# Kernel optimization log

Measured on AMD Instinct MI355X. Metric: run time of the kernel, lower is better.

## Reference

```python
import jax, jax.numpy as jnp
import numpy as np

B, D, H = 512, 256, 512

def setup_inputs() -> dict:
    key = jax.random.key(0)
    ks = jax.random.split(key, 7)
    s = lambda fan_in: 1.0 / np.sqrt(fan_in)
    return {
        "h": jax.random.normal(ks[0], (B, D), jnp.float32),
        "W1": jax.random.normal(ks[1], (2 * D, H), jnp.float32) * s(2 * D),
        "b1": jax.random.normal(ks[2], (H,), jnp.float32) * s(2 * D),
        "W2": jax.random.normal(ks[3], (H, H), jnp.float32) * s(H),
        "b2": jax.random.normal(ks[4], (H,), jnp.float32) * s(H),
        "W3": jax.random.normal(ks[5], (H, 1), jnp.float32) * s(H),
        "b3": jax.random.normal(ks[6], (1,), jnp.float32) * s(H),
    }

def reference(h, W1, b1, W2, b2, W3, b3):
    n = h.shape[0]
    # Split W1 into halves acting on hi and hj; equivalent to cat([hi,hj]) @ W1
    yi = h @ W1[:D]            # [B, H]
    yj = h @ W1[D:]            # [B, H]
    x = jnp.tanh(yi[:, None, :] + yj[None, :, :] + b1)   # [B, B, H]
    x = jnp.tanh(x @ W2 + b2)                             # [B, B, H]
    logits = (x @ W3 + b3)[..., 0]                        # [B, B]
    eye = jnp.eye(n, dtype=logits.dtype)
    return logits * (1.0 - eye) + (-20.0) * eye
```

## Files before the change

kernel.cpp:

```cpp
#include <hip/hip_runtime.h>
#include <hip/hip_bf16.h>
#include <cstdint>


#define NB 512
#define ND 256
#define NH 512
#define C2 2.885390081777927f

typedef int i32x4 __attribute__((ext_vector_type(4)));
typedef int i32x16 __attribute__((ext_vector_type(16)));
typedef unsigned int u32;
typedef unsigned char u8;

__device__ __forceinline__ float exp2_fast(float x) {
#if __has_builtin(__builtin_amdgcn_exp2f)
  return __builtin_amdgcn_exp2f(x);
#else
  return exp2f(x);
#endif
}
__device__ __forceinline__ float rcp_fast(float x) {
#if __has_builtin(__builtin_amdgcn_rcpf)
  return __builtin_amdgcn_rcpf(x);
#else
  return 1.0f / x;
#endif
}
__device__ __forceinline__ u32 perm_b32(u32 hi, u32 lo, u32 sel) {
#if __has_builtin(__builtin_amdgcn_perm)
  return __builtin_amdgcn_perm(hi, lo, sel);
#else
  u32 r = 0;
  for (int b = 0; b < 4; ++b) {
    const u32 c = (sel >> (8 * b)) & 255;
    const u32 byte = (c < 4) ? (lo >> (8 * c)) & 255 : (c < 8) ? (hi >> (8 * (c - 4))) & 255 : 0;
    r |= byte << (8 * b);
  }
  return r;
#endif
}
__device__ __forceinline__ u32 tanh_q127_magic(float u) {
  const float r = rcp_fast(exp2_fast(u) + 1.0f);
  return __builtin_bit_cast(u32, fmaf(-254.0f, r, 12583039.0f));
}

__global__ __launch_bounds__(256) void prep_all(const float* __restrict__ h,
                                                const float* __restrict__ W1,
                                                const float* __restrict__ b1,
                                                const float* __restrict__ W2,
                                                float* __restrict__ Ai,
                                                float* __restrict__ Aj,
                                                u8* __restrict__ W2q) {
  const int t = threadIdx.x;
  const int bx = blockIdx.x;
  if (bx < 1024) {
    __shared__ float hsh[ND];
    const int i = bx >> 1;
    const int n = (bx & 1) * 256 + t;
    hsh[t] = h[i * ND + t];
    __syncthreads();
    float ai = 0.0f, aj = 0.0f;
#pragma unroll 8
    for (int d = 0; d < ND; ++d) {
      const float hd = hsh[d];
      ai = fmaf(hd, W1[d * NH + n], ai);
      aj = fmaf(hd, W1[(d + ND) * NH + n], aj);
    }
    Ai[i * NH + n] = ai * C2;
    Aj[i * NH + n] = (aj + b1[n]) * C2;
  } else {
    const int g = (bx - 1024) * 256 + t;
    const int lane = g & 63;
    const int nt = (g >> 6) & 15;
    const int ks = g >> 10;
    const int n = nt * 32 + (lane & 31);
    const int kb = ks * 32 + ((lane >> 5) << 4);
    u32 w[4];
#pragma unroll
    for (int q = 0; q < 4; ++q) {
      u32 acc = 0;
#pragma unroll
      for (int j = 0; j < 4; ++j) {
        const float wv = fminf(fmaxf(W2[(kb + q * 4 + j) * NH + n], -0.25f), 0.25f);
        const int qi = (int)rintf(wv * 508.0f);
        acc |= ((u32)(qi & 255)) << (8 * j);
      }
      w[q] = acc;
    }
    ((uint4*)W2q)[g] = make_uint4(w[0], w[1], w[2], w[3]);
  }
}

__global__ __launch_bounds__(512, 6) void pair_main(const float* __restrict__ Ai,
                                                    const float* __restrict__ Aj,
                                                    const u8* __restrict__ W2q,
                                                    const float* __restrict__ b2,
                                                    const float* __restrict__ W3,
                                                    const float* __restrict__ b3,
                                                    float* __restrict__ out) {
  __shared__ __align__(16) u8 xs[32 * 512];
  __shared__ float red[8][32];

  const int t = threadIdx.x;
  const int w = t >> 6;
  const int lane = t & 63;
  const int lhi = lane >> 5;
  const int llo = lane & 31;
  const int bx = blockIdx.x;
  const int i = bx >> 4;
  const int j0 = (bx & 15) * 32;

  i32x16 acc[2];
#pragma unroll
  for (int nt = 0; nt < 2; ++nt)
#pragma unroll
    for (int q = 0; q < 16; ++q) acc[nt][q] = 0;

  {
    const int row = t & 31;
    const int s0 = t >> 5;
    const float* ajr = Aj + (size_t)(j0 + row) * NH;
    const float* air = Ai + (size_t)i * NH;
#pragma unroll
    for (int uu = 0; uu < 2; ++uu) {
      const int s = s0 + uu * 16;
      const int k0 = s * 16;
      u32 wds[4];
#pragma unroll
      for (int q = 0; q < 4; ++q) {
        const float4 fa = *(const float4*)(ajr + k0 + q * 4);
        const float4 ga = *(const float4*)(air + k0 + q * 4);
        const u32 m0 = tanh_q127_magic(fa.x + ga.x);
        const u32 m1 = tanh_q127_magic(fa.y + ga.y);
        const u32 m2 = tanh_q127_magic(fa.z + ga.z);
        const u32 m3 = tanh_q127_magic(fa.w + ga.w);
        const u32 p01 = perm_b32(m1, m0, 0x0C0C0400u);
        const u32 p23 = perm_b32(m3, m2, 0x0C0C0400u);
        wds[q] = perm_b32(p23, p01, 0x05040100u);
      }
      ((uint4*)xs)[s * 32 + row] = make_uint4(wds[0], wds[1], wds[2], wds[3]);
    }
  }
  __syncthreads();

  const i32x4* xsv = (const i32x4*)xs;
  const int abase = lhi * 32 + llo;
  const uint4* w2v = (const uint4*)W2q + w * 128 + lane;

  i32x4 aP0 = xsv[abase];
  i32x4 aP1 = xsv[64 + abase];
  uint4 bP00 = w2v[0], bP01 = w2v[64];
  uint4 bP10 = w2v[1024], bP11 = w2v[1024 + 64];

#pragma unroll
  for (int kk = 0; kk < 8; ++kk) {
    const int ks0 = 2 * kk;
    {
      const i32x4 a = aP0;
      const i32x4 c0 = __builtin_bit_cast(i32x4, bP00);
      const i32x4 c1 = __builtin_bit_cast(i32x4, bP01);
      if (kk < 7) {
        aP0 = xsv[(ks0 + 2) * 64 + abase];
        const uint4* wp = w2v + (ks0 + 2) * 1024;
        bP00 = wp[0];
        bP01 = wp[64];
      }
      acc[0] = __builtin_amdgcn_mfma_i32_32x32x32_i8(a, c0, acc[0], 0, 0, 0);
      acc[1] = __builtin_amdgcn_mfma_i32_32x32x32_i8(a, c1, acc[1], 0, 0, 0);
    }
    {
      const i32x4 a = aP1;
      const i32x4 c0 = __builtin_bit_cast(i32x4, bP10);
      const i32x4 c1 = __builtin_bit_cast(i32x4, bP11);
      if (kk < 7) {
        aP1 = xsv[(ks0 + 3) * 64 + abase];
        const uint4* wp = w2v + (ks0 + 3) * 1024;
        bP10 = wp[0];
        bP11 = wp[64];
      }
      acc[0] = __builtin_amdgcn_mfma_i32_32x32x32_i8(a, c0, acc[0], 0, 0, 0);
      acc[1] = __builtin_amdgcn_mfma_i32_32x32x32_i8(a, c1, acc[1], 0, 0, 0);
    }
  }

  const float SCALE = (0.25f / (127.0f * 127.0f)) * C2;
  float b2c[2], w3v[2];
#pragma unroll
  for (int ntl = 0; ntl < 2; ++ntl) {
    const int n = w * 64 + ntl * 32 + llo;
    b2c[ntl] = b2[n] * C2;
    w3v[ntl] = W3[n];
  }
  float w3s = w3v[0] + w3v[1];
#pragma unroll
  for (int off = 1; off < 32; off <<= 1) w3s += __shfl_xor(w3s, off, 64);

#pragma unroll
  for (int reg = 0; reg < 16; ++reg) {
    float sr = 0.0f;
#pragma unroll
    for (int ntl = 0; ntl < 2; ++ntl) {
      const float y = fmaf((float)acc[ntl][reg], SCALE, b2c[ntl]);
      const float r = rcp_fast(exp2_fast(y) + 1.0f);
      sr = fmaf(w3v[ntl], r, sr);
    }
#pragma unroll
    for (int off = 1; off < 32; off <<= 1) sr += __shfl_xor(sr, off, 64);
    const int row = (reg & 3) + 8 * (reg >> 2) + 4 * lhi;
    if (llo == reg) red[w][row] = fmaf(-2.0f, sr, w3s);
  }
  __syncthreads();
  if (t < 32) {
    float v = b3[0];
#pragma unroll
    for (int ww = 0; ww < 8; ++ww) v += red[ww][t];
    const int j = j0 + t;
    out[i * NB + j] = (j == i) ? -20.0f : v;
  }
}

extern "C" void kernel_launch(void* const* d_in, const int* in_sizes, int n_in,
                              void* d_out, int out_size, void* d_ws, size_t ws_size,
                              hipStream_t stream) {
  const float* h = (const float*)d_in[0];
  const float* W1 = (const float*)d_in[1];
  const float* b1 = (const float*)d_in[2];
  const float* W2 = (const float*)d_in[3];
  const float* b2 = (const float*)d_in[4];
  const float* W3 = (const float*)d_in[5];
  const float* b3 = (const float*)d_in[6];
  float* out = (float*)d_out;

  float* Ai = (float*)d_ws;
  float* Aj = Ai + NB * NH;
  u8* W2q = (u8*)(Aj + NB * NH);

  prep_all<<<1088, 256, 0, stream>>>(h, W1, b1, W2, Ai, Aj, W2q);
  pair_main<<<8192, 512, 0, stream>>>(Ai, Aj, W2q, b2, W3, b3, out);
}
```

Before: 233.6 us.

## Enlarge pair tiles to 64 rows and batch four rows in W1 prep

pair_main now uses 1024-thread blocks that each cover 64 j-rows. Two groups of 8 waves share the same W2q column slices, which halves the grid and the per-block overhead. prep_all computes four h rows per block so each W1 element loaded is reused four times. The larger blocks raise the LDS per block and the launch bounds may pressure registers, which could lower occupancy or cause spills.

```diff
diff --git a/kernel.cpp b/kernel.cpp
--- a/kernel.cpp
+++ b/kernel.cpp
@@ -1,5 +1,4 @@
 #include <hip/hip_runtime.h>
-#include <hip/hip_bf16.h>
 #include <cstdint>
 
 
@@ -54,23 +53,34 @@
                                                 u8* __restrict__ W2q) {
   const int t = threadIdx.x;
   const int bx = blockIdx.x;
-  if (bx < 1024) {
-    __shared__ float hsh[ND];
-    const int i = bx >> 1;
+  if (bx < 256) {
+    __shared__ float hsh[4][ND];
+    const int i0 = (bx >> 1) * 4;
     const int n = (bx & 1) * 256 + t;
-    hsh[t] = h[i * ND + t];
+#pragma unroll
+    for (int ii = 0; ii < 4; ++ii) hsh[ii][t] = h[(i0 + ii) * ND + t];
     __syncthreads();
-    float ai = 0.0f, aj = 0.0f;
-#pragma unroll 8
+    float ai[4] = {0.0f, 0.0f, 0.0f, 0.0f};
+    float aj[4] = {0.0f, 0.0f, 0.0f, 0.0f};
+#pragma unroll 4
     for (int d = 0; d < ND; ++d) {
-      const float hd = hsh[d];
-      ai = fmaf(hd, W1[d * NH + n], ai);
-      aj = fmaf(hd, W1[(d + ND) * NH + n], aj);
-    }
-    Ai[i * NH + n] = ai * C2;
-    Aj[i * NH + n] = (aj + b1[n]) * C2;
+      const float wa = W1[d * NH + n];
+      const float wb = W1[(d + ND) * NH + n];
+#pragma unroll
+      for (int ii = 0; ii < 4; ++ii) {
+        const float hd = hsh[ii][d];
+        ai[ii] = fmaf(hd, wa, ai[ii]);
+        aj[ii] = fmaf(hd, wb, aj[ii]);
+      }
+    }
+    const float b1n = b1[n];
+#pragma unroll
+    for (int ii = 0; ii < 4; ++ii) {
+      Ai[(i0 + ii) * NH + n] = ai[ii] * C2;
+      Aj[(i0 + ii) * NH + n] = (aj[ii] + b1n) * C2;
+    }
   } else {
-    const int g = (bx - 1024) * 256 + t;
+    const int g = (bx - 256) * 256 + t;
     const int lane = g & 63;
     const int nt = (g >> 6) & 15;
     const int ks = g >> 10;
@@ -92,24 +102,26 @@
   }
 }
 
-__global__ __launch_bounds__(512, 6) void pair_main(const float* __restrict__ Ai,
-                                                    const float* __restrict__ Aj,
-                                                    const u8* __restrict__ W2q,
-                                                    const float* __restrict__ b2,
-                                                    const float* __restrict__ W3,
-                                                    const float* __restrict__ b3,
-                                                    float* __restrict__ out) {
-  __shared__ __align__(16) u8 xs[32 * 512];
-  __shared__ float red[8][32];
+__global__ __launch_bounds__(1024, 8) void pair_main(const float* __restrict__ Ai,
+                                                     const float* __restrict__ Aj,
+                                                     const u8* __restrict__ W2q,
+                                                     const float* __restrict__ b2,
+                                                     const float* __restrict__ W3,
+                                                     const float* __restrict__ b3,
+                                                     float* __restrict__ out) {
+  __shared__ __align__(16) u8 xs[64 * 512];
+  __shared__ float red[16][32];
 
   const int t = threadIdx.x;
   const int w = t >> 6;
   const int lane = t & 63;
   const int lhi = lane >> 5;
   const int llo = lane & 31;
+  const int wn = w & 7;
+  const int mh = w >> 3;
   const int bx = blockIdx.x;
-  const int i = bx >> 4;
-  const int j0 = (bx & 15) * 32;
+  const int i = bx >> 3;
+  const int j0 = (bx & 7) * 64;
 
   i32x16 acc[2];
 #pragma unroll
@@ -118,8 +130,8 @@
     for (int q = 0; q < 16; ++q) acc[nt][q] = 0;
 
   {
-    const int row = t & 31;
-    const int s0 = t >> 5;
+    const int row = t & 63;
+    const int s0 = t >> 6;
     const float* ajr = Aj + (size_t)(j0 + row) * NH;
     const float* air = Ai + (size_t)i * NH;
 #pragma unroll
@@ -139,17 +151,17 @@
         const u32 p23 = perm_b32(m3, m2, 0x0C0C0400u);
         wds[q] = perm_b32(p23, p01, 0x05040100u);
       }
-      ((uint4*)xs)[s * 32 + row] = make_uint4(wds[0], wds[1], wds[2], wds[3]);
+      ((uint4*)xs)[s * 64 + row] = make_uint4(wds[0], wds[1], wds[2], wds[3]);
     }
   }
   __syncthreads();
 
   const i32x4* xsv = (const i32x4*)xs;
-  const int abase = lhi * 32 + llo;
-  const uint4* w2v = (const uint4*)W2q + w * 128 + lane;
+  const int abase = lhi * 64 + mh * 32 + llo;
+  const uint4* w2v = (const uint4*)W2q + wn * 128 + lane;
 
   i32x4 aP0 = xsv[abase];
-  i32x4 aP1 = xsv[64 + abase];
+  i32x4 aP1 = xsv[128 + abase];
   uint4 bP00 = w2v[0], bP01 = w2v[64];
   uint4 bP10 = w2v[1024], bP11 = w2v[1024 + 64];
 
@@ -161,7 +173,7 @@
       const i32x4 c0 = __builtin_bit_cast(i32x4, bP00);
       const i32x4 c1 = __builtin_bit_cast(i32x4, bP01);
       if (kk < 7) {
-        aP0 = xsv[(ks0 + 2) * 64 + abase];
+        aP0 = xsv[(ks0 + 2) * 128 + abase];
         const uint4* wp = w2v + (ks0 + 2) * 1024;
         bP00 = wp[0];
         bP01 = wp[64];
@@ -174,7 +186,7 @@
       const i32x4 c0 = __builtin_bit_cast(i32x4, bP10);
       const i32x4 c1 = __builtin_bit_cast(i32x4, bP11);
       if (kk < 7) {
-        aP1 = xsv[(ks0 + 3) * 64 + abase];
+        aP1 = xsv[(ks0 + 3) * 128 + abase];
         const uint4* wp = w2v + (ks0 + 3) * 1024;
         bP10 = wp[0];
         bP11 = wp[64];
@@ -188,7 +200,7 @@
   float b2c[2], w3v[2];
 #pragma unroll
   for (int ntl = 0; ntl < 2; ++ntl) {
-    const int n = w * 64 + ntl * 32 + llo;
+    const int n = wn * 64 + ntl * 32 + llo;
     b2c[ntl] = b2[n] * C2;
     w3v[ntl] = W3[n];
   }
@@ -211,10 +223,12 @@
     if (llo == reg) red[w][row] = fmaf(-2.0f, sr, w3s);
   }
   __syncthreads();
-  if (t < 32) {
+  if (t < 64) {
+    const int mh2 = t >> 5;
+    const int rl = t & 31;
     float v = b3[0];
 #pragma unroll
-    for (int ww = 0; ww < 8; ++ww) v += red[ww][t];
+    for (int ww = 0; ww < 8; ++ww) v += red[mh2 * 8 + ww][rl];
     const int j = j0 + t;
     out[i * NB + j] = (j == i) ? -20.0f : v;
   }
@@ -236,6 +250,6 @@
   float* Aj = Ai + NB * NH;
   u8* W2q = (u8*)(Aj + NB * NH);
 
-  prep_all<<<1088, 256, 0, stream>>>(h, W1, b1, W2, Ai, Aj, W2q);
-  pair_main<<<8192, 512, 0, stream>>>(Ai, Aj, W2q, b2, W3, b3, out);
-}
+  prep_all<<<320, 256, 0, stream>>>(h, W1, b1, W2, Ai, Aj, W2q);
+  pair_main<<<4096, 1024, 0, stream>>>(Ai, Aj, W2q, b2, W3, b3, out);
+}
```

Result: slower. 248.2 us (+6.3%).

## Make pair kernel persistent per row with double-buffered tanh tile overlap

Applied to the files above, without the earlier changes.

Each pair_main block now owns one row i and loops over all 16 column tiles. The tanh quantization of the next tile's activations is computed and written into a second shared-memory buffer, interleaved with the current tile's int8 MFMA steps, with Aj rows prefetched into registers. The reduction output is also double-buffered to drop one barrier per tile. The prep kernel's W1 projection becomes a shared-memory tiled GEMM (16 rows by 32 columns per block), which raises W1 reuse. The trade-off is a grid cut from 8192 to 512 blocks, lower occupancy bounds and higher register pressure, so latency hiding depends on the intra-block overlap.

```diff
diff --git a/kernel.cpp b/kernel.cpp
--- a/kernel.cpp
+++ b/kernel.cpp
@@ -1,5 +1,4 @@
 #include <hip/hip_runtime.h>
-#include <hip/hip_bf16.h>
 #include <cstdint>
 
 
@@ -54,23 +53,59 @@
                                                 u8* __restrict__ W2q) {
   const int t = threadIdx.x;
   const int bx = blockIdx.x;
-  if (bx < 1024) {
-    __shared__ float hsh[ND];
-    const int i = bx >> 1;
-    const int n = (bx & 1) * 256 + t;
-    hsh[t] = h[i * ND + t];
-    __syncthreads();
-    float ai = 0.0f, aj = 0.0f;
-#pragma unroll 8
-    for (int d = 0; d < ND; ++d) {
-      const float hd = hsh[d];
-      ai = fmaf(hd, W1[d * NH + n], ai);
-      aj = fmaf(hd, W1[(d + ND) * NH + n], aj);
-    }
-    Ai[i * NH + n] = ai * C2;
-    Aj[i * NH + n] = (aj + b1[n]) * C2;
+  if (bx < 512) {
+    __shared__ float hs[16][68];
+    __shared__ float w1t[64][36];
+    __shared__ float w1b[64][36];
+    const int it = bx >> 4, nt = bx & 15;
+    const int i0 = it * 16, n0 = nt * 32;
+    const int nn = t & 31, ig = t >> 5;
+    float accA[2] = {0.f, 0.f}, accB[2] = {0.f, 0.f};
+    for (int c2 = 0; c2 < 4; ++c2) {
+      __syncthreads();
+      {
+        const int r = t >> 4, c0 = (t & 15) * 4;
+        *(float4*)&hs[r][c0] = *(const float4*)(h + (size_t)(i0 + r) * ND + c2 * 64 + c0);
+      }
+      {
+        const int r = t >> 2, c0 = (t & 3) * 8;
+        const float* st = W1 + (size_t)(c2 * 64 + r) * NH + n0 + c0;
+        const float* sb = W1 + (size_t)(256 + c2 * 64 + r) * NH + n0 + c0;
+        const float4 a = *(const float4*)st;
+        const float4 b = *(const float4*)(st + 4);
+        const float4 c = *(const float4*)sb;
+        const float4 d = *(const float4*)(sb + 4);
+        *(float4*)&w1t[r][c0] = a;
+        *(float4*)&w1t[r][c0 + 4] = b;
+        *(float4*)&w1b[r][c0] = c;
+        *(float4*)&w1b[r][c0 + 4] = d;
+      }
+      __syncthreads();
+#pragma unroll 4
+      for (int k4 = 0; k4 < 16; ++k4) {
+        const float4 hv0 = *(const float4*)&hs[ig * 2 + 0][k4 * 4];
+        const float4 hv1 = *(const float4*)&hs[ig * 2 + 1][k4 * 4];
+        const float* h0 = (const float*)&hv0;
+        const float* h1 = (const float*)&hv1;
+#pragma unroll
+        for (int j = 0; j < 4; ++j) {
+          const float wtj = w1t[k4 * 4 + j][nn];
+          const float wbj = w1b[k4 * 4 + j][nn];
+          accA[0] = fmaf(h0[j], wtj, accA[0]);
+          accA[1] = fmaf(h1[j], wtj, accA[1]);
+          accB[0] = fmaf(h0[j], wbj, accB[0]);
+          accB[1] = fmaf(h1[j], wbj, accB[1]);
+        }
+      }
+    }
+    const float b1n = b1[n0 + nn];
+#pragma unroll
+    for (int r = 0; r < 2; ++r) {
+      Ai[(size_t)(i0 + ig * 2 + r) * NH + n0 + nn] = accA[r] * C2;
+      Aj[(size_t)(i0 + ig * 2 + r) * NH + n0 + nn] = (accB[r] + b1n) * C2;
+    }
   } else {
-    const int g = (bx - 1024) * 256 + t;
+    const int g = (bx - 512) * 256 + t;
     const int lane = g & 63;
     const int nt = (g >> 6) & 15;
     const int ks = g >> 10;
@@ -92,40 +127,45 @@
   }
 }
 
-__global__ __launch_bounds__(512, 6) void pair_main(const float* __restrict__ Ai,
+__global__ __launch_bounds__(512, 4) void pair_main(const float* __restrict__ Ai,
                                                     const float* __restrict__ Aj,
                                                     const u8* __restrict__ W2q,
                                                     const float* __restrict__ b2,
                                                     const float* __restrict__ W3,
                                                     const float* __restrict__ b3,
                                                     float* __restrict__ out) {
-  __shared__ __align__(16) u8 xs[32 * 512];
-  __shared__ float red[8][32];
+  __shared__ __align__(16) u8 xs[2][32 * 512];
+  __shared__ float red[2][8][32];
 
   const int t = threadIdx.x;
   const int w = t >> 6;
   const int lane = t & 63;
   const int lhi = lane >> 5;
   const int llo = lane & 31;
-  const int bx = blockIdx.x;
-  const int i = bx >> 4;
-  const int j0 = (bx & 15) * 32;
-
-  i32x16 acc[2];
-#pragma unroll
-  for (int nt = 0; nt < 2; ++nt)
-#pragma unroll
-    for (int q = 0; q < 16; ++q) acc[nt][q] = 0;
+  const int i = blockIdx.x;
+
+  const int srow = t & 31;
+  const int ss0 = t >> 5;
+  const float* air = Ai + (size_t)i * NH;
+
+  const float SCALE = (0.25f / (127.0f * 127.0f)) * C2;
+  float b2c[2], w3v[2];
+#pragma unroll
+  for (int ntl = 0; ntl < 2; ++ntl) {
+    const int n = w * 64 + ntl * 32 + llo;
+    b2c[ntl] = b2[n] * C2;
+    w3v[ntl] = W3[n];
+  }
+  float w3s = w3v[0] + w3v[1];
+#pragma unroll
+  for (int off = 1; off < 32; off <<= 1) w3s += __shfl_xor(w3s, off, 64);
+  const float b3v = b3[0];
 
   {
-    const int row = t & 31;
-    const int s0 = t >> 5;
-    const float* ajr = Aj + (size_t)(j0 + row) * NH;
-    const float* air = Ai + (size_t)i * NH;
+    const float* ajr = Aj + (size_t)srow * NH;
 #pragma unroll
     for (int uu = 0; uu < 2; ++uu) {
-      const int s = s0 + uu * 16;
-      const int k0 = s * 16;
+      const int k0 = ss0 * 16 + uu * 256;
       u32 wds[4];
 #pragma unroll
       for (int q = 0; q < 4; ++q) {
@@ -139,84 +179,126 @@
         const u32 p23 = perm_b32(m3, m2, 0x0C0C0400u);
         wds[q] = perm_b32(p23, p01, 0x05040100u);
       }
-      ((uint4*)xs)[s * 32 + row] = make_uint4(wds[0], wds[1], wds[2], wds[3]);
+      ((uint4*)xs[0])[(ss0 + uu * 16) * 32 + srow] = make_uint4(wds[0], wds[1], wds[2], wds[3]);
+    }
+  }
+  float4 fjv[8];
+  {
+    const float* ajn = Aj + (size_t)(32 + srow) * NH;
+#pragma unroll
+    for (int g = 0; g < 8; ++g) {
+      const int koff = ss0 * 16 + (g >> 2) * 256 + (g & 3) * 4;
+      fjv[g] = *(const float4*)(ajn + koff);
     }
   }
   __syncthreads();
 
-  const i32x4* xsv = (const i32x4*)xs;
   const int abase = lhi * 32 + llo;
   const uint4* w2v = (const uint4*)W2q + w * 128 + lane;
 
-  i32x4 aP0 = xsv[abase];
-  i32x4 aP1 = xsv[64 + abase];
-  uint4 bP00 = w2v[0], bP01 = w2v[64];
-  uint4 bP10 = w2v[1024], bP11 = w2v[1024 + 64];
-
-#pragma unroll
-  for (int kk = 0; kk < 8; ++kk) {
-    const int ks0 = 2 * kk;
-    {
-      const i32x4 a = aP0;
-      const i32x4 c0 = __builtin_bit_cast(i32x4, bP00);
-      const i32x4 c1 = __builtin_bit_cast(i32x4, bP01);
-      if (kk < 7) {
-        aP0 = xsv[(ks0 + 2) * 64 + abase];
-        const uint4* wp = w2v + (ks0 + 2) * 1024;
-        bP00 = wp[0];
-        bP01 = wp[64];
-      }
-      acc[0] = __builtin_amdgcn_mfma_i32_32x32x32_i8(a, c0, acc[0], 0, 0, 0);
-      acc[1] = __builtin_amdgcn_mfma_i32_32x32x32_i8(a, c1, acc[1], 0, 0, 0);
-    }
-    {
-      const i32x4 a = aP1;
-      const i32x4 c0 = __builtin_bit_cast(i32x4, bP10);
-      const i32x4 c1 = __builtin_bit_cast(i32x4, bP11);
-      if (kk < 7) {
-        aP1 = xsv[(ks0 + 3) * 64 + abase];
-        const uint4* wp = w2v + (ks0 + 3) * 1024;
-        bP10 = wp[0];
-        bP11 = wp[64];
-      }
-      acc[0] = __builtin_amdgcn_mfma_i32_32x32x32_i8(a, c0, acc[0], 0, 0, 0);
-      acc[1] = __builtin_amdgcn_mfma_i32_32x32x32_i8(a, c1, acc[1], 0, 0, 0);
-    }
-  }
-
-  const float SCALE = (0.25f / (127.0f * 127.0f)) * C2;
-  float b2c[2], w3v[2];
-#pragma unroll
-  for (int ntl = 0; ntl < 2; ++ntl) {
-    const int n = w * 64 + ntl * 32 + llo;
-    b2c[ntl] = b2[n] * C2;
-    w3v[ntl] = W3[n];
-  }
-  float w3s = w3v[0] + w3v[1];
-#pragma unroll
-  for (int off = 1; off < 32; off <<= 1) w3s += __shfl_xor(w3s, off, 64);
-
-#pragma unroll
-  for (int reg = 0; reg < 16; ++reg) {
-    float sr = 0.0f;
-#pragma unroll
-    for (int ntl = 0; ntl < 2; ++ntl) {
-      const float y = fmaf((float)acc[ntl][reg], SCALE, b2c[ntl]);
-      const float r = rcp_fast(exp2_fast(y) + 1.0f);
-      sr = fmaf(w3v[ntl], r, sr);
-    }
-#pragma unroll
-    for (int off = 1; off < 32; off <<= 1) sr += __shfl_xor(sr, off, 64);
-    const int row = (reg & 3) + 8 * (reg >> 2) + 4 * lhi;
-    if (llo == reg) red[w][row] = fmaf(-2.0f, sr, w3s);
-  }
-  __syncthreads();
+#pragma unroll 1
+  for (int p = 0; p < 16; ++p) {
+    const i32x4* xsv = (const i32x4*)xs[p & 1];
+    u8* xsw = xs[(p + 1) & 1];
+    const bool notlast = (p < 15);
+
+    i32x16 acc[2];
+#pragma unroll
+    for (int nt = 0; nt < 2; ++nt)
+#pragma unroll
+      for (int q = 0; q < 16; ++q) acc[nt][q] = 0;
+
+    i32x4 aP0 = xsv[abase];
+    i32x4 aP1 = xsv[64 + abase];
+    uint4 bP00 = w2v[0], bP01 = w2v[64];
+    uint4 bP10 = w2v[1024], bP11 = w2v[1024 + 64];
+
+    u32 wd[8];
+#pragma unroll
+    for (int kk = 0; kk < 8; ++kk) {
+      const int ks0 = 2 * kk;
+      {
+        const i32x4 a = aP0;
+        const i32x4 c0 = __builtin_bit_cast(i32x4, bP00);
+        const i32x4 c1 = __builtin_bit_cast(i32x4, bP01);
+        if (kk < 7) {
+          aP0 = xsv[(ks0 + 2) * 64 + abase];
+          const uint4* wp = w2v + (ks0 + 2) * 1024;
+          bP00 = wp[0];
+          bP01 = wp[64];
+        }
+        acc[0] = __builtin_amdgcn_mfma_i32_32x32x32_i8(a, c0, acc[0], 0, 0, 0);
+        acc[1] = __builtin_amdgcn_mfma_i32_32x32x32_i8(a, c1, acc[1], 0, 0, 0);
+      }
+      if (notlast) {
+        const int koff = ss0 * 16 + (kk >> 2) * 256 + (kk & 3) * 4;
+        const float4 ga = *(const float4*)(air + koff);
+        const float4 fa = fjv[kk];
+        const u32 m0 = tanh_q127_magic(fa.x + ga.x);
+        const u32 m1 = tanh_q127_magic(fa.y + ga.y);
+        const u32 m2 = tanh_q127_magic(fa.z + ga.z);
+        const u32 m3 = tanh_q127_magic(fa.w + ga.w);
+        const u32 p01 = perm_b32(m1, m0, 0x0C0C0400u);
+        const u32 p23 = perm_b32(m3, m2, 0x0C0C0400u);
+        wd[kk] = perm_b32(p23, p01, 0x05040100u);
+        if (kk == 3) ((uint4*)xsw)[ss0 * 32 + srow] = make_uint4(wd[0], wd[1], wd[2], wd[3]);
+        if (kk == 7) ((uint4*)xsw)[(ss0 + 16) * 32 + srow] = make_uint4(wd[4], wd[5], wd[6], wd[7]);
+      }
+      {
+        const i32x4 a = aP1;
+        const i32x4 c0 = __builtin_bit_cast(i32x4, bP10);
+        const i32x4 c1 = __builtin_bit_cast(i32x4, bP11);
+        if (kk < 7) {
+          aP1 = xsv[(ks0 + 3) * 64 + abase];
+          const uint4* wp = w2v + (ks0 + 3) * 1024;
+          bP10 = wp[0];
+          bP11 = wp[64];
+        }
+        acc[0] = __builtin_amdgcn_mfma_i32_32x32x32_i8(a, c0, acc[0], 0, 0, 0);
+        acc[1] = __builtin_amdgcn_mfma_i32_32x32x32_i8(a, c1, acc[1], 0, 0, 0);
+      }
+    }
+
+    if (p < 14) {
+      const float* ajn = Aj + (size_t)((p + 2) * 32 + srow) * NH;
+#pragma unroll
+      for (int g = 0; g < 8; ++g) {
+        const int koff = ss0 * 16 + (g >> 2) * 256 + (g & 3) * 4;
+        fjv[g] = *(const float4*)(ajn + koff);
+      }
+    }
+
+#pragma unroll
+    for (int reg = 0; reg < 16; ++reg) {
+      float sr = 0.0f;
+#pragma unroll
+      for (int ntl = 0; ntl < 2; ++ntl) {
+        const float y = fmaf((float)acc[ntl][reg], SCALE, b2c[ntl]);
+        const float r = rcp_fast(exp2_fast(y) + 1.0f);
+        sr = fmaf(w3v[ntl], r, sr);
+      }
+#pragma unroll
+      for (int off = 1; off < 32; off <<= 1) sr += __shfl_xor(sr, off, 64);
+      const int row = (reg & 3) + 8 * (reg >> 2) + 4 * lhi;
+      if (llo == reg) red[p & 1][w][row] = fmaf(-2.0f, sr, w3s);
+    }
+
+    if (p > 0 && t < 32) {
+      float v = b3v;
+#pragma unroll
+      for (int ww = 0; ww < 8; ++ww) v += red[(p & 1) ^ 1][ww][t];
+      const int jp = (p - 1) * 32 + t;
+      out[i * NB + jp] = (jp == i) ? -20.0f : v;
+    }
+    __syncthreads();
+  }
+
   if (t < 32) {
-    float v = b3[0];
-#pragma unroll
-    for (int ww = 0; ww < 8; ++ww) v += red[ww][t];
-    const int j = j0 + t;
-    out[i * NB + j] = (j == i) ? -20.0f : v;
+    float v = b3v;
+#pragma unroll
+    for (int ww = 0; ww < 8; ++ww) v += red[1][ww][t];
+    const int jp = 480 + t;
+    out[i * NB + jp] = (jp == i) ? -20.0f : v;
   }
 }
 
@@ -236,6 +318,6 @@
   float* Aj = Ai + NB * NH;
   u8* W2q = (u8*)(Aj + NB * NH);
 
-  prep_all<<<1088, 256, 0, stream>>>(h, W1, b1, W2, Ai, Aj, W2q);
-  pair_main<<<8192, 512, 0, stream>>>(Ai, Aj, W2q, b2, W3, b3, out);
-}
+  prep_all<<<576, 256, 0, stream>>>(h, W1, b1, W2, Ai, Aj, W2q);
+  pair_main<<<512, 512, 0, stream>>>(Ai, Aj, W2q, b2, W3, b3, out);
+}
```

After: 430.1 us. 84.1% more time.

## Tile first-layer projection in prep kernel with shared-memory staging of h and W1

Applied to the files above, without the earlier changes.

Replaces the per-row projection, where each block streamed all of W1 from global memory for a single input row, with a tiled GEMM. Each block now computes a 16x32 output tile and stages h and both W1 halves through shared memory in 64-wide K chunks. This cuts global W1 traffic by reusing each loaded weight across 16 rows, and halves the number of prep blocks. The prep kernel is small next to pair_main, so the effect on total time is limited.

```diff
diff --git a/kernel.cpp b/kernel.cpp
--- a/kernel.cpp
+++ b/kernel.cpp
@@ -1,5 +1,4 @@
 #include <hip/hip_runtime.h>
-#include <hip/hip_bf16.h>
 #include <cstdint>
 
 
@@ -54,23 +53,59 @@
                                                 u8* __restrict__ W2q) {
   const int t = threadIdx.x;
   const int bx = blockIdx.x;
-  if (bx < 1024) {
-    __shared__ float hsh[ND];
-    const int i = bx >> 1;
-    const int n = (bx & 1) * 256 + t;
-    hsh[t] = h[i * ND + t];
-    __syncthreads();
-    float ai = 0.0f, aj = 0.0f;
-#pragma unroll 8
-    for (int d = 0; d < ND; ++d) {
-      const float hd = hsh[d];
-      ai = fmaf(hd, W1[d * NH + n], ai);
-      aj = fmaf(hd, W1[(d + ND) * NH + n], aj);
-    }
-    Ai[i * NH + n] = ai * C2;
-    Aj[i * NH + n] = (aj + b1[n]) * C2;
+  if (bx < 512) {
+    __shared__ float hs[16][68];
+    __shared__ float w1t[64][36];
+    __shared__ float w1b[64][36];
+    const int it = bx >> 4, nt = bx & 15;
+    const int i0 = it * 16, n0 = nt * 32;
+    const int nn = t & 31, ig = t >> 5;
+    float accA[2] = {0.f, 0.f}, accB[2] = {0.f, 0.f};
+    for (int c2 = 0; c2 < 4; ++c2) {
+      __syncthreads();
+      {
+        const int r = t >> 4, c0 = (t & 15) * 4;
+        *(float4*)&hs[r][c0] = *(const float4*)(h + (size_t)(i0 + r) * ND + c2 * 64 + c0);
+      }
+      {
+        const int r = t >> 2, c0 = (t & 3) * 8;
+        const float* st = W1 + (size_t)(c2 * 64 + r) * NH + n0 + c0;
+        const float* sb = W1 + (size_t)(256 + c2 * 64 + r) * NH + n0 + c0;
+        const float4 a = *(const float4*)st;
+        const float4 b = *(const float4*)(st + 4);
+        const float4 c = *(const float4*)sb;
+        const float4 d = *(const float4*)(sb + 4);
+        *(float4*)&w1t[r][c0] = a;
+        *(float4*)&w1t[r][c0 + 4] = b;
+        *(float4*)&w1b[r][c0] = c;
+        *(float4*)&w1b[r][c0 + 4] = d;
+      }
+      __syncthreads();
+#pragma unroll 4
+      for (int k4 = 0; k4 < 16; ++k4) {
+        const float4 hv0 = *(const float4*)&hs[ig * 2 + 0][k4 * 4];
+        const float4 hv1 = *(const float4*)&hs[ig * 2 + 1][k4 * 4];
+        const float* h0 = (const float*)&hv0;
+        const float* h1 = (const float*)&hv1;
+#pragma unroll
+        for (int j = 0; j < 4; ++j) {
+          const float wtj = w1t[k4 * 4 + j][nn];
+          const float wbj = w1b[k4 * 4 + j][nn];
+          accA[0] = fmaf(h0[j], wtj, accA[0]);
+          accA[1] = fmaf(h1[j], wtj, accA[1]);
+          accB[0] = fmaf(h0[j], wbj, accB[0]);
+          accB[1] = fmaf(h1[j], wbj, accB[1]);
+        }
+      }
+    }
+    const float b1n = b1[n0 + nn];
+#pragma unroll
+    for (int r = 0; r < 2; ++r) {
+      Ai[(size_t)(i0 + ig * 2 + r) * NH + n0 + nn] = accA[r] * C2;
+      Aj[(size_t)(i0 + ig * 2 + r) * NH + n0 + nn] = (accB[r] + b1n) * C2;
+    }
   } else {
-    const int g = (bx - 1024) * 256 + t;
+    const int g = (bx - 512) * 256 + t;
     const int lane = g & 63;
     const int nt = (g >> 6) & 15;
     const int ks = g >> 10;
@@ -236,6 +271,6 @@
   float* Aj = Ai + NB * NH;
   u8* W2q = (u8*)(Aj + NB * NH);
 
-  prep_all<<<1088, 256, 0, stream>>>(h, W1, b1, W2, Ai, Aj, W2q);
+  prep_all<<<576, 256, 0, stream>>>(h, W1, b1, W2, Ai, Aj, W2q);
   pair_main<<<8192, 512, 0, stream>>>(Ai, Aj, W2q, b2, W3, b3, out);
 }
```

After: 225.5 us. 3.5% less time.
